# Kernel optimization log

Hardware: AMD Instinct MI355X
Metric: run time of the kernel (lower is better)

## Reference

```python
import jax, jax.numpy as jnp
import numpy as np

DM = 512      # d_model
DM4 = DM // 4 # per-modality embed dim
DI = 2 * DM   # d_inner (expand=2)
DS = 16       # d_state
DTR = 32      # dt_rank = d_model/16
DC = 4        # d_conv
NL = 3        # n_layers
SD = 17       # state_dim
AD = 7        # act_dim
MAXT = 2048   # max_ep_len
EPS = 1e-5


def setup_inputs() -> dict:
    key = jax.random.key(0)
    ks = jax.random.split(key, 32)
    B, L = 2, 1024
    f32 = jnp.float32

    def rn(k, shape, s=0.02):
        return jax.random.normal(k, shape, f32) * s

    inp = {}
    inp["states"] = jax.random.normal(ks[0], (B, L, SD), f32)
    inp["actions"] = jax.random.normal(ks[1], (B, L, AD), f32)
    inp["returns_to_go"] = jax.random.normal(ks[2], (B, L, 1), f32)
    inp["constraints_to_go"] = jax.random.normal(ks[3], (B, L, 1), f32)
    inp["timesteps"] = jax.random.randint(ks[4], (B, L), 0, MAXT)

    # embedding heads
    inp["W_s"] = rn(ks[5], (DM4, SD)); inp["b_s"] = jnp.zeros((DM4,), f32)
    inp["W_a"] = rn(ks[6], (DM4, AD)); inp["b_a"] = jnp.zeros((DM4,), f32)
    inp["W_r"] = rn(ks[7], (DM4, 1));  inp["b_r"] = jnp.zeros((DM4,), f32)
    inp["W_c"] = rn(ks[8], (DM4, 1));  inp["b_c"] = jnp.zeros((DM4,), f32)
    inp["E_t"] = rn(ks[9], (MAXT, DM4))

    # per-layer Mamba params (stacked on leading layer dim)
    inp["ln_g"] = jnp.ones((NL, DM), f32)
    inp["ln_b"] = jnp.zeros((NL, DM), f32)
    inp["in_w"] = rn(ks[10], (NL, 2 * DI, DM))
    inp["conv_w"] = rn(ks[11], (NL, DI, DC), 0.1)
    inp["conv_b"] = jnp.zeros((NL, DI), f32)
    inp["xproj_w"] = rn(ks[12], (NL, DTR + 2 * DS, DI))
    inp["dtproj_w"] = rn(ks[13], (NL, DI, DTR), 0.1)
    inp["dtproj_b"] = jnp.full((NL, DI), -4.6, f32)  # softplus^-1(~0.01)
    inp["A_log"] = jnp.log(jnp.broadcast_to(jnp.arange(1, DS + 1, dtype=f32), (NL, DI, DS)))
    inp["D_ssm"] = jnp.ones((NL, DI), f32)
    inp["out_w"] = rn(ks[14], (NL, DM, DI))

    inp["fn_g"] = jnp.ones((DM,), f32)
    inp["fn_b"] = jnp.zeros((DM,), f32)
    inp["W_ps"] = rn(ks[15], (SD, DM4)); inp["b_ps"] = jnp.zeros((SD,), f32)
    inp["W_pa"] = rn(ks[16], (AD, DM4)); inp["b_pa"] = jnp.zeros((AD,), f32)
    return inp


def _layernorm(x, g, b):
    mu = x.mean(-1, keepdims=True)
    v = ((x - mu) ** 2).mean(-1, keepdims=True)
    return (x - mu) * jax.lax.rsqrt(v + EPS) * g + b


def _mamba_mixer(x, in_w, conv_w, conv_b, xproj_w, dtproj_w, dtproj_b, A_log, Dv, out_w):
    B, L, _ = x.shape
    xz = jnp.einsum('bld,ed->ble', x, in_w)          # (B,L,2*DI)
    xc, z = jnp.split(xz, 2, axis=-1)
    # causal depthwise conv1d, kernel DC
    xp = jnp.pad(xc, ((0, 0), (DC - 1, 0), (0, 0)))
    xc = sum(xp[:, k:k + L, :] * conv_w[:, k] for k in range(DC)) + conv_b
    xc = jax.nn.silu(xc)
    xdbl = jnp.einsum('bld,ed->ble', xc, xproj_w)    # (B,L,DTR+2*DS)
    dt_low = xdbl[..., :DTR]
    Bm = xdbl[..., DTR:DTR + DS]
    Cm = xdbl[..., DTR + DS:]
    dt = jax.nn.softplus(jnp.einsum('blr,dr->bld', dt_low, dtproj_w) + dtproj_b)
    A = -jnp.exp(A_log)                               # (DI,DS)

    def step(h, xs):
        dt_t, B_t, C_t, u_t = xs                      # (B,DI),(B,DS),(B,DS),(B,DI)
        dA = jnp.exp(dt_t[:, :, None] * A)            # (B,DI,DS)
        h = h * dA + (dt_t * u_t)[:, :, None] * B_t[:, None, :]
        y = jnp.einsum('bds,bs->bd', h, C_t)
        return h, y

    h0 = jnp.zeros((B, DI, DS), x.dtype)
    xs = (dt.transpose(1, 0, 2), Bm.transpose(1, 0, 2), Cm.transpose(1, 0, 2), xc.transpose(1, 0, 2))
    _, ys = jax.lax.scan(step, h0, xs)               # (L,B,DI)
    y = ys.transpose(1, 0, 2) + Dv * xc
    y = y * jax.nn.silu(z)
    return jnp.einsum('bld,ed->ble', y, out_w)


def reference(states, actions, returns_to_go, constraints_to_go, timesteps,
              W_s, b_s, W_a, b_a, W_r, b_r, W_c, b_c, E_t,
              ln_g, ln_b, in_w, conv_w, conv_b, xproj_w, dtproj_w, dtproj_b,
              A_log, D_ssm, out_w, fn_g, fn_b, W_ps, b_ps, W_pa, b_pa):
    B, L = timesteps.shape
    te = E_t[timesteps]                               # (B,L,DM4)
    se = states @ W_s.T + b_s + te
    ae = actions @ W_a.T + b_a + te
    re = returns_to_go @ W_r.T + b_r + te
    ce = constraints_to_go @ W_c.T + b_c + te
    # shift actions right by one, zero at t=0
    ae = jnp.concatenate([jnp.zeros_like(ae[:, :1]), ae[:, :-1]], axis=1)
    x = jnp.stack((re, ce, se, ae), axis=2).reshape(B, L, 4 * DM4)  # (B,L,DM)
    for i in range(NL):
        x = x + _mamba_mixer(_layernorm(x, ln_g[i], ln_b[i]),
                             in_w[i], conv_w[i], conv_b[i], xproj_w[i],
                             dtproj_w[i], dtproj_b[i], A_log[i], D_ssm[i], out_w[i])
    x = _layernorm(x, fn_g, fn_b)
    out = x.reshape(B, L, 4, DM4)
    state_preds = out[:, :, 3] @ W_ps.T + b_ps
    action_preds = out[:, :, 2] @ W_pa.T + b_pa
    return (state_preds, action_preds)
```

## Files before the change

kernel.cpp:

```cpp
#include <hip/hip_runtime.h>
#include <cstdint>
#include <cstddef>

#define DMf 512
#define DM4 128
#define DIi 1024
#define DSs 16
#define DTRr 32
#define NLl 3
#define SDd 17
#define ADd 7
#define Bb 2
#define Ll 1024
#define NTOK (Bb*Ll)
#define CL 32
#define NCH 32

typedef __bf16 bf16x8 __attribute__((ext_vector_type(8)));
typedef float f32x4 __attribute__((ext_vector_type(4)));

__device__ inline unsigned short f2bf(float f){
  unsigned int u = __float_as_uint(f);
  unsigned int r = (u + 0x7FFFu + ((u>>16)&1u)) >> 16;
  return (unsigned short)r;
}
__device__ inline float silu_f(float v){ return v / (1.0f + __expf(-v)); }

__global__ __launch_bounds__(256) void cast_bf16_k(const float* __restrict__ src,
    unsigned short* __restrict__ dst, int n){
  int i = blockIdx.x*256 + threadIdx.x;
  if (i < n) dst[i] = f2bf(src[i]);
}

__global__ __launch_bounds__(128) void embed_k(
    const float* __restrict__ st, const float* __restrict__ ac,
    const float* __restrict__ rtg, const float* __restrict__ ctg,
    const int* __restrict__ ts,
    const float* __restrict__ Ws, const float* __restrict__ bs,
    const float* __restrict__ Wa, const float* __restrict__ ba,
    const float* __restrict__ Wr, const float* __restrict__ br,
    const float* __restrict__ Wc, const float* __restrict__ bc,
    const float* __restrict__ Et, float* __restrict__ x)
{
  int tok = blockIdx.x; int j = threadIdx.x;
  int l = tok & (Ll-1);
  int t = ts[tok];
  float te = Et[(size_t)t*DM4 + j];
  float re = rtg[tok]*Wr[j] + br[j] + te;
  float ce = ctg[tok]*Wc[j] + bc[j] + te;
  float se = bs[j] + te;
  #pragma unroll
  for (int k=0;k<SDd;++k) se += st[(size_t)tok*SDd+k]*Ws[j*SDd+k];
  float ae = 0.0f;
  if (l > 0) {
    int tp = ts[tok-1];
    ae = ba[j] + Et[(size_t)tp*DM4 + j];
    #pragma unroll
    for (int k=0;k<ADd;++k) ae += ac[(size_t)(tok-1)*ADd+k]*Wa[j*ADd+k];
  }
  float* xt = x + (size_t)tok*DMf;
  xt[0*DM4+j]=re; xt[1*DM4+j]=ce; xt[2*DM4+j]=se; xt[3*DM4+j]=ae;
}

__global__ __launch_bounds__(256) void ln_k(const float* __restrict__ x,
    const float* __restrict__ g, const float* __restrict__ bta,
    unsigned short* __restrict__ xn)
{
  int wave = threadIdx.x >> 6, lane = threadIdx.x & 63;
  int tok = blockIdx.x*4 + wave;
  const float* xr = x + (size_t)tok*DMf;
  float v[8];
  float4 a = *(const float4*)&xr[lane*8];
  float4 b = *(const float4*)&xr[lane*8+4];
  v[0]=a.x; v[1]=a.y; v[2]=a.z; v[3]=a.w; v[4]=b.x; v[5]=b.y; v[6]=b.z; v[7]=b.w;
  float s = 0.f;
  #pragma unroll
  for (int j=0;j<8;++j) s += v[j];
  #pragma unroll
  for (int m=32;m>=1;m>>=1) s += __shfl_xor(s, m, 64);
  float mu = s * (1.0f/DMf);
  float vs = 0.f;
  #pragma unroll
  for (int j=0;j<8;++j){ float d = v[j]-mu; vs += d*d; }
  #pragma unroll
  for (int m=32;m>=1;m>>=1) vs += __shfl_xor(vs, m, 64);
  float rstd = rsqrtf(vs*(1.0f/DMf) + 1e-5f);
  unsigned int o[8];
  #pragma unroll
  for (int j=0;j<8;++j){
    int c = lane*8+j;
    o[j] = f2bf((v[j]-mu)*rstd*g[c] + bta[c]);
  }
  uint4 w;
  w.x = o[0] | (o[1]<<16); w.y = o[2] | (o[3]<<16);
  w.z = o[4] | (o[5]<<16); w.w = o[6] | (o[7]<<16);
  *(uint4*)&xn[(size_t)tok*DMf + lane*8] = w;
}

template<int ACCUM>
__global__ __launch_bounds__(256) void gemm_bt_k(const unsigned short* __restrict__ A,
    const unsigned short* __restrict__ Bm, float* __restrict__ C, int M, int N, int K)
{
  __shared__ unsigned short As[128*32];
  __shared__ unsigned short Bs[128*32];
  int tid = threadIdx.x;
  int bm = blockIdx.x, bn = blockIdx.y;
  size_t row0 = (size_t)bm*128, col0 = (size_t)bn*128;
  int wave = tid>>6, lane = tid&63;
  int wr = wave>>1, wc = wave&1;
  f32x4 acc[4][4];
  f32x4 z4 = {0.f,0.f,0.f,0.f};
  #pragma unroll
  for (int m=0;m<4;++m)
    #pragma unroll
    for (int n=0;n<4;++n) acc[m][n] = z4;
  int lrow = lane&15, lko = (lane>>4)*8;
  for (int k0=0; k0<K; k0+=32){
    #pragma unroll
    for (int r=0;r<2;++r){
      int flat = r*256 + tid;
      int arow = flat>>2, ak = (flat&3)*8;
      const unsigned short* ga = A + (row0+arow)*K + k0 + ak;
      const unsigned short* gb = Bm + (col0+arow)*K + k0 + ak;
      __builtin_amdgcn_global_load_lds((const __attribute__((address_space(1))) void*)ga,
          (__attribute__((address_space(3))) void*)(&As[flat*8]), 16, 0, 0);
      __builtin_amdgcn_global_load_lds((const __attribute__((address_space(1))) void*)gb,
          (__attribute__((address_space(3))) void*)(&Bs[flat*8]), 16, 0, 0);
    }
    __syncthreads();
    bf16x8 af[4], bfv[4];
    #pragma unroll
    for (int m=0;m<4;++m) af[m] = *(const bf16x8*)&As[(wr*64+m*16+lrow)*32 + lko];
    #pragma unroll
    for (int n=0;n<4;++n) bfv[n] = *(const bf16x8*)&Bs[(wc*64+n*16+lrow)*32 + lko];
    #pragma unroll
    for (int m=0;m<4;++m)
      #pragma unroll
      for (int n=0;n<4;++n)
        acc[m][n] = __builtin_amdgcn_mfma_f32_16x16x32_bf16(af[m], bfv[n], acc[m][n], 0, 0, 0);
    __syncthreads();
  }
  int lcol = lane&15, lr4 = (lane>>4)*4;
  #pragma unroll
  for (int m=0;m<4;++m)
    #pragma unroll
    for (int n=0;n<4;++n){
      size_t row = row0 + wr*64 + m*16 + lr4;
      size_t col = col0 + wc*64 + n*16 + lcol;
      #pragma unroll
      for (int j=0;j<4;++j){
        float vv = acc[m][n][j];
        float* p = &C[(row+j)*N + col];
        if (ACCUM) *p += vv; else *p = vv;
      }
    }
}

__global__ __launch_bounds__(256) void gemm_bt64_k(const unsigned short* __restrict__ A,
    const unsigned short* __restrict__ Bm, float* __restrict__ C, int M, int N, int K)
{
  __shared__ unsigned short As[64*32];
  __shared__ unsigned short Bs[64*32];
  int tid = threadIdx.x;
  size_t row0 = (size_t)blockIdx.x*64, col0 = (size_t)blockIdx.y*64;
  int wave = tid>>6, lane = tid&63;
  int wr = wave>>1, wc = wave&1;
  f32x4 acc[2][2];
  f32x4 z4 = {0.f,0.f,0.f,0.f};
  acc[0][0]=z4; acc[0][1]=z4; acc[1][0]=z4; acc[1][1]=z4;
  int lrow = lane&15, lko = (lane>>4)*8;
  int srow = tid>>2, sk = (tid&3)*8;
  for (int k0=0; k0<K; k0+=32){
    const unsigned short* ga = A + (row0+srow)*K + k0 + sk;
    const unsigned short* gb = Bm + (col0+srow)*K + k0 + sk;
    __builtin_amdgcn_global_load_lds((const __attribute__((address_space(1))) void*)ga,
        (__attribute__((address_space(3))) void*)(&As[tid*8]), 16, 0, 0);
    __builtin_amdgcn_global_load_lds((const __attribute__((address_space(1))) void*)gb,
        (__attribute__((address_space(3))) void*)(&Bs[tid*8]), 16, 0, 0);
    __syncthreads();
    bf16x8 af[2], bfv[2];
    #pragma unroll
    for (int m=0;m<2;++m) af[m] = *(const bf16x8*)&As[(wr*32+m*16+lrow)*32 + lko];
    #pragma unroll
    for (int n=0;n<2;++n) bfv[n] = *(const bf16x8*)&Bs[(wc*32+n*16+lrow)*32 + lko];
    #pragma unroll
    for (int m=0;m<2;++m)
      #pragma unroll
      for (int n=0;n<2;++n)
        acc[m][n] = __builtin_amdgcn_mfma_f32_16x16x32_bf16(af[m], bfv[n], acc[m][n], 0, 0, 0);
    __syncthreads();
  }
  int lcol = lane&15, lr4 = (lane>>4)*4;
  #pragma unroll
  for (int m=0;m<2;++m)
    #pragma unroll
    for (int n=0;n<2;++n){
      size_t row = row0 + wr*32 + m*16 + lr4;
      size_t col = col0 + wc*32 + n*16 + lcol;
      #pragma unroll
      for (int j=0;j<4;++j)
        C[(row+j)*N + col] += acc[m][n][j];
    }
}

__global__ __launch_bounds__(256) void conv_k(const float* __restrict__ xz,
    const float* __restrict__ cw, const float* __restrict__ cb,
    float* __restrict__ xc, unsigned short* __restrict__ xcbf)
{
  int idx = blockIdx.x*256 + threadIdx.x;
  int d = idx & (DIi-1); int tok = idx >> 10; int l = tok & (Ll-1);
  float acc = cb[d];
  #pragma unroll
  for (int k=0;k<4;++k){
    int ll = l + k - 3;
    if (ll >= 0) acc += xz[(size_t)(tok + k - 3)*(2*DIi) + d] * cw[d*4+k];
  }
  float v = silu_f(acc);
  xc[idx] = v;
  xcbf[idx] = f2bf(v);
}

__global__ __launch_bounds__(256) void xproj_mfma_k(const unsigned short* __restrict__ A,
    const unsigned short* __restrict__ Bw, float* __restrict__ xdbl)
{
  __shared__ unsigned short As[64*32];
  __shared__ unsigned short Bs[64*32];
  int tid = threadIdx.x;
  size_t row0 = (size_t)blockIdx.x*64;
  int wave = tid>>6, lane = tid&63;
  int wr = wave>>1, wc = wave&1;
  f32x4 acc[2][2];
  f32x4 z4 = {0.f,0.f,0.f,0.f};
  acc[0][0]=z4; acc[0][1]=z4; acc[1][0]=z4; acc[1][1]=z4;
  int lrow = lane&15, lko = (lane>>4)*8;
  int srow = tid>>2, sk = (tid&3)*8;
  for (int k0=0; k0<DIi; k0+=32){
    const unsigned short* ga = A + (row0+srow)*DIi + k0 + sk;
    const unsigned short* gb = Bw + (size_t)srow*DIi + k0 + sk;
    __builtin_amdgcn_global_load_lds((const __attribute__((address_space(1))) void*)ga,
        (__attribute__((address_space(3))) void*)(&As[tid*8]), 16, 0, 0);
    __builtin_amdgcn_global_load_lds((const __attribute__((address_space(1))) void*)gb,
        (__attribute__((address_space(3))) void*)(&Bs[tid*8]), 16, 0, 0);
    __syncthreads();
    bf16x8 af[2], bfv[2];
    #pragma unroll
    for (int m=0;m<2;++m) af[m] = *(const bf16x8*)&As[(wr*32+m*16+lrow)*32 + lko];
    #pragma unroll
    for (int n=0;n<2;++n) bfv[n] = *(const bf16x8*)&Bs[(wc*32+n*16+lrow)*32 + lko];
    #pragma unroll
    for (int m=0;m<2;++m)
      #pragma unroll
      for (int n=0;n<2;++n)
        acc[m][n] = __builtin_amdgcn_mfma_f32_16x16x32_bf16(af[m], bfv[n], acc[m][n], 0, 0, 0);
    __syncthreads();
  }
  int lcol = lane&15, lr4 = (lane>>4)*4;
  #pragma unroll
  for (int m=0;m<2;++m)
    #pragma unroll
    for (int n=0;n<2;++n){
      size_t row = row0 + wr*32 + m*16 + lr4;
      int col = wc*32 + n*16 + lcol;
      #pragma unroll
      for (int j=0;j<4;++j)
        xdbl[(row+j)*64 + col] = acc[m][n][j];
    }
}

__global__ __launch_bounds__(256) void dtproj_k(const float* __restrict__ xdbl,
    const float* __restrict__ dw, const float* __restrict__ db, float* __restrict__ dt)
{
  int bid = blockIdx.x;
  int tok0 = (bid >> 2) * 8;
  int o = (bid & 3)*256 + threadIdx.x;
  __shared__ float lows[8][32];
  {
    int tt = threadIdx.x >> 5, kk = threadIdx.x & 31;
    lows[tt][kk] = xdbl[(size_t)(tok0+tt)*64 + kk];
  }
  __syncthreads();
  float w[32];
  #pragma unroll
  for (int q=0;q<8;++q)
    *(float4*)&w[q*4] = *(const float4*)&dw[(size_t)o*32 + q*4];
  float bias = db[o];
  #pragma unroll
  for (int t=0;t<8;++t){
    float acc = bias;
    #pragma unroll
    for (int k=0;k<32;++k) acc += w[k]*lows[t][k];
    float dv = (acc > 15.0f) ? acc : log1pf(__expf(acc));
    dt[(size_t)(tok0+t)*DIi + o] = dv;
  }
}

__global__ __launch_bounds__(256) void scan1_k(const float* __restrict__ dt,
    const float* __restrict__ xc, const float* __restrict__ xdbl,
    const float* __restrict__ Alog, float* __restrict__ Ebuf, float* __restrict__ Pbuf)
{
  int bid = blockIdx.x;
  int dblk = bid & 3; int tmp = bid >> 2; int c = tmp & (NCH-1); int b = tmp >> 5;
  int d = dblk*256 + threadIdx.x;
  float A[16], h[16], P[16];
  #pragma unroll
  for (int s=0;s<16;++s){ A[s] = -__expf(Alog[d*16+s]); h[s]=0.f; P[s]=1.f; }
  int l0 = c*CL;
  for (int l=l0; l<l0+CL; ++l){
    size_t tok = (size_t)b*Ll + l;
    float dtv = dt[tok*DIi + d];
    float u   = xc[tok*DIi + d];
    float dtu = dtv*u;
    const float* bcv = &xdbl[tok*64 + 32];
    #pragma unroll
    for (int s=0;s<16;++s){
      float dA = __expf(dtv*A[s]);
      h[s] = h[s]*dA + dtu*bcv[s];
      P[s] *= dA;
    }
  }
  size_t base = (((size_t)b*DIi + d)*NCH + c)*16;
  #pragma unroll
  for (int s=0;s<16;++s){ Ebuf[base+s]=h[s]; Pbuf[base+s]=P[s]; }
}

__global__ __launch_bounds__(256) void scanmid_k(const float* __restrict__ E,
    const float* __restrict__ P, float* __restrict__ H0)
{
  int gid = blockIdx.x*256 + threadIdx.x;
  int s = gid & 15; size_t bd = (size_t)(gid >> 4);
  float H = 0.f;
  for (int c=0;c<NCH;++c){
    size_t idx = (bd*NCH + c)*16 + s;
    H0[idx] = H;
    H = P[idx]*H + E[idx];
  }
}

__global__ __launch_bounds__(256) void scan2_k(const float* __restrict__ dt,
    const float* __restrict__ xc, const float* __restrict__ xdbl,
    const float* __restrict__ Alog, const float* __restrict__ Dv,
    const float* __restrict__ xz, const float* __restrict__ H0,
    unsigned short* __restrict__ ybf)
{
  int bid = blockIdx.x;
  int dblk = bid & 3; int tmp = bid >> 2; int c = tmp & (NCH-1); int b = tmp >> 5;
  int d = dblk*256 + threadIdx.x;
  size_t base = (((size_t)b*DIi + d)*NCH + c)*16;
  float A[16], h[16];
  #pragma unroll
  for (int s=0;s<16;++s){ A[s] = -__expf(Alog[d*16+s]); h[s] = H0[base+s]; }
  float Dd = Dv[d];
  int l0 = c*CL;
  for (int l=l0; l<l0+CL; ++l){
    size_t tok = (size_t)b*Ll + l;
    float dtv = dt[tok*DIi + d];
    float u   = xc[tok*DIi + d];
    float dtu = dtv*u;
    const float* bcv = &xdbl[tok*64 + 32];
    float y = 0.f;
    #pragma unroll
    for (int s=0;s<16;++s){
      float dA = __expf(dtv*A[s]);
      h[s] = h[s]*dA + dtu*bcv[s];
      y += h[s]*bcv[16+s];
    }
    float zv = xz[tok*(2*DIi) + DIi + d];
    ybf[tok*DIi + d] = f2bf((y + Dd*u) * silu_f(zv));
  }
}

__global__ __launch_bounds__(256) void head_k(const float* __restrict__ x,
    const float* __restrict__ g, const float* __restrict__ bta,
    const float* __restrict__ Wps, const float* __restrict__ bps,
    const float* __restrict__ Wpa, const float* __restrict__ bpa,
    float* __restrict__ out)
{
  __shared__ float lds[4][256];
  int wave = threadIdx.x >> 6, lane = threadIdx.x & 63;
  int tok = blockIdx.x*4 + wave;
  const float* xr = x + (size_t)tok*DMf;
  float v[8];
  float4 a = *(const float4*)&xr[lane*8];
  float4 b = *(const float4*)&xr[lane*8+4];
  v[0]=a.x; v[1]=a.y; v[2]=a.z; v[3]=a.w; v[4]=b.x; v[5]=b.y; v[6]=b.z; v[7]=b.w;
  float s = 0.f;
  #pragma unroll
  for (int j=0;j<8;++j) s += v[j];
  #pragma unroll
  for (int m=32;m>=1;m>>=1) s += __shfl_xor(s, m, 64);
  float mu = s * (1.0f/DMf);
  float vs = 0.f;
  #pragma unroll
  for (int j=0;j<8;++j){ float d = v[j]-mu; vs += d*d; }
  #pragma unroll
  for (int m=32;m>=1;m>>=1) vs += __shfl_xor(vs, m, 64);
  float rstd = rsqrtf(vs*(1.0f/DMf) + 1e-5f);
  if (lane >= 32){
    #pragma unroll
    for (int j=0;j<8;++j){
      int cdx = lane*8+j;
      lds[wave][cdx-256] = (v[j]-mu)*rstd*g[cdx] + bta[cdx];
    }
  }
  __syncthreads();
  if (lane < SDd){
    float acc = bps[lane];
    const float* w = &Wps[lane*DM4];
    #pragma unroll 8
    for (int k=0;k<DM4;++k) acc += lds[wave][128+k]*w[k];
    out[(size_t)tok*SDd + lane] = acc;
  } else if (lane < SDd+ADd){
    int o = lane - SDd;
    float acc = bpa[o];
    const float* w = &Wpa[o*DM4];
    #pragma unroll 8
    for (int k=0;k<DM4;++k) acc += lds[wave][k]*w[k];
    out[(size_t)NTOK*SDd + (size_t)tok*ADd + o] = acc;
  }
}

extern "C" void kernel_launch(void* const* d_in, const int* in_sizes, int n_in,
                              void* d_out, int out_size, void* d_ws, size_t ws_size,
                              hipStream_t stream)
{
  (void)in_sizes; (void)n_in; (void)out_size;
  const float* states   = (const float*)d_in[0];
  const float* actions  = (const float*)d_in[1];
  const float* rtg      = (const float*)d_in[2];
  const float* ctg      = (const float*)d_in[3];
  const int*   ts       = (const int*)d_in[4];
  const float* W_s      = (const float*)d_in[5];
  const float* b_s      = (const float*)d_in[6];
  const float* W_a      = (const float*)d_in[7];
  const float* b_a      = (const float*)d_in[8];
  const float* W_r      = (const float*)d_in[9];
  const float* b_r      = (const float*)d_in[10];
  const float* W_c      = (const float*)d_in[11];
  const float* b_c      = (const float*)d_in[12];
  const float* E_t      = (const float*)d_in[13];
  const float* ln_g     = (const float*)d_in[14];
  const float* ln_b     = (const float*)d_in[15];
  const float* in_w     = (const float*)d_in[16];
  const float* conv_w   = (const float*)d_in[17];
  const float* conv_b   = (const float*)d_in[18];
  const float* xproj_w  = (const float*)d_in[19];
  const float* dtproj_w = (const float*)d_in[20];
  const float* dtproj_b = (const float*)d_in[21];
  const float* A_log    = (const float*)d_in[22];
  const float* D_ssm    = (const float*)d_in[23];
  const float* out_w    = (const float*)d_in[24];
  const float* fn_g     = (const float*)d_in[25];
  const float* fn_b     = (const float*)d_in[26];
  const float* W_ps     = (const float*)d_in[27];
  const float* b_ps     = (const float*)d_in[28];
  const float* W_pa     = (const float*)d_in[29];
  const float* b_pa     = (const float*)d_in[30];

  char* ws = (char*)d_ws;
  constexpr size_t S_X    = (size_t)NTOK*DMf*4;
  constexpr size_t S_XN   = (size_t)NTOK*DMf*2;
  constexpr size_t S_XZ   = (size_t)NTOK*2*DIi*4;
  constexpr size_t S_XC   = (size_t)NTOK*DIi*4;
  constexpr size_t S_XCB  = (size_t)NTOK*DIi*2;
  constexpr size_t S_XDBL = (size_t)NTOK*64*4;
  constexpr size_t S_DT   = (size_t)NTOK*DIi*4;
  constexpr size_t S_YBF  = (size_t)NTOK*DIi*2;
  constexpr size_t S_INW  = (size_t)NLl*2048*512*2;
  constexpr size_t S_OUTW = (size_t)NLl*512*1024*2;
  constexpr size_t S_XPW  = (size_t)NLl*64*DIi*2;
  constexpr size_t S_E    = (size_t)Bb*DIi*NCH*16*4;
  constexpr size_t S_TOTAL = S_X+S_XN+S_XZ+S_XC+S_XCB+S_XDBL+S_DT+S_YBF
                             +S_INW+S_OUTW+S_XPW+3*S_E;

  if (ws_size < S_TOTAL) return;

  size_t off = 0;
  float* x            = (float*)(ws + off);          off += S_X;
  unsigned short* xn  = (unsigned short*)(ws + off); off += S_XN;
  float* xz           = (float*)(ws + off);          off += S_XZ;
  float* xc           = (float*)(ws + off);          off += S_XC;
  unsigned short* xcbf= (unsigned short*)(ws + off); off += S_XCB;
  float* xdbl         = (float*)(ws + off);          off += S_XDBL;
  float* dt           = (float*)(ws + off);          off += S_DT;
  unsigned short* ybf = (unsigned short*)(ws + off); off += S_YBF;
  unsigned short* inw_bf  = (unsigned short*)(ws + off); off += S_INW;
  unsigned short* outw_bf = (unsigned short*)(ws + off); off += S_OUTW;
  unsigned short* xpw_bf  = (unsigned short*)(ws + off); off += S_XPW;
  float* Ebuf         = (float*)(ws + off);          off += S_E;
  float* Pbuf         = (float*)(ws + off);          off += S_E;
  float* H0buf        = (float*)(ws + off);          off += S_E;

  const int n_inw  = NLl*2048*512;
  const int n_outw = NLl*512*1024;
  const int n_xpw  = NLl*64*DIi;
  cast_bf16_k<<<(n_inw+255)/256, 256, 0, stream>>>(in_w, inw_bf, n_inw);
  cast_bf16_k<<<(n_outw+255)/256, 256, 0, stream>>>(out_w, outw_bf, n_outw);
  cast_bf16_k<<<(n_xpw+255)/256, 256, 0, stream>>>(xproj_w, xpw_bf, n_xpw);

  embed_k<<<NTOK, 128, 0, stream>>>(states, actions, rtg, ctg, ts,
      W_s, b_s, W_a, b_a, W_r, b_r, W_c, b_c, E_t, x);

  for (int i=0;i<NLl;++i){
    ln_k<<<NTOK/4, 256, 0, stream>>>(x, ln_g + i*DMf, ln_b + i*DMf, xn);
    gemm_bt_k<0><<<dim3(NTOK/128, 2048/128), 256, 0, stream>>>(
        xn, inw_bf + (size_t)i*2048*512, xz, NTOK, 2048, 512);
    conv_k<<<(NTOK*DIi)/256, 256, 0, stream>>>(xz, conv_w + (size_t)i*DIi*4,
        conv_b + (size_t)i*DIi, xc, xcbf);
    xproj_mfma_k<<<NTOK/64, 256, 0, stream>>>(xcbf, xpw_bf + (size_t)i*64*DIi, xdbl);
    dtproj_k<<<(NTOK/8)*4, 256, 0, stream>>>(xdbl, dtproj_w + (size_t)i*DIi*32,
        dtproj_b + (size_t)i*DIi, dt);
    scan1_k<<<Bb*NCH*4, 256, 0, stream>>>(dt, xc, xdbl,
        A_log + (size_t)i*DIi*16, Ebuf, Pbuf);
    scanmid_k<<<(Bb*DIi*16)/256, 256, 0, stream>>>(Ebuf, Pbuf, H0buf);
    scan2_k<<<Bb*NCH*4, 256, 0, stream>>>(dt, xc, xdbl,
        A_log + (size_t)i*DIi*16, D_ssm + (size_t)i*DIi, xz, H0buf, ybf);
    gemm_bt64_k<<<dim3(NTOK/64, 512/64), 256, 0, stream>>>(
        ybf, outw_bf + (size_t)i*512*1024, x, NTOK, 512, 1024);
  }

  head_k<<<NTOK/4, 256, 0, stream>>>(x, fn_g, fn_b, W_ps, b_ps, W_pa, b_pa,
      (float*)d_out);
}
```

Baseline: 385.5 us.

## Fuse dt projection into scan kernels, double-buffer GEMM tiles, merge weight casts

Removes the separate dtproj kernel and the dt buffer by recomputing the dt projection and softplus inside both scan passes, so the NTOK x DI dt array is never written or re-read. All three MFMA GEMM kernels gain double-buffered LDS with explicit waitcnt and barrier-based prefetch of the next K slice, overlapping loads with compute. The three weight-cast launches merge into one kernel, and the scan chunk length halves (CL 16, NCH 64) for more parallel blocks. The trade-off is that the dt projection is computed twice, and the scan carry buffers double in size.

```diff
diff --git a/kernel.cpp b/kernel.cpp
--- a/kernel.cpp
+++ b/kernel.cpp
@@ -13,8 +13,8 @@
 #define Bb 2
 #define Ll 1024
 #define NTOK (Bb*Ll)
-#define CL 32
-#define NCH 32
+#define CL 16
+#define NCH 64
 
 typedef __bf16 bf16x8 __attribute__((ext_vector_type(8)));
 typedef float f32x4 __attribute__((ext_vector_type(4)));
@@ -26,10 +26,16 @@
 }
 __device__ inline float silu_f(float v){ return v / (1.0f + __expf(-v)); }
 
-__global__ __launch_bounds__(256) void cast_bf16_k(const float* __restrict__ src,
-    unsigned short* __restrict__ dst, int n){
+__global__ __launch_bounds__(256) void cast3_k(
+    const float* __restrict__ a, unsigned short* __restrict__ da, int na,
+    const float* __restrict__ b, unsigned short* __restrict__ db, int nb,
+    const float* __restrict__ c, unsigned short* __restrict__ dc, int nc){
   int i = blockIdx.x*256 + threadIdx.x;
-  if (i < n) dst[i] = f2bf(src[i]);
+  if (i < na) { da[i] = f2bf(a[i]); return; }
+  int j = i - na;
+  if (j < nb) { db[j] = f2bf(b[j]); return; }
+  int k = j - nb;
+  if (k < nc) dc[k] = f2bf(c[k]);
 }
 
 __global__ __launch_bounds__(128) void embed_k(
@@ -97,15 +103,27 @@
   *(uint4*)&xn[(size_t)tok*DMf + lane*8] = w;
 }
 
+#define STAGE128(buf, kk) { \
+  _Pragma("unroll") \
+  for (int r=0;r<2;++r){ \
+    int flat = r*256 + tid; \
+    int arow = flat>>2, ak = (flat&3)*8; \
+    const unsigned short* ga = A + (row0+arow)*K + (kk) + ak; \
+    const unsigned short* gb = Bm + (col0+arow)*K + (kk) + ak; \
+    __builtin_amdgcn_global_load_lds((const __attribute__((address_space(1))) void*)ga, \
+        (__attribute__((address_space(3))) void*)(&As[buf][flat*8]), 16, 0, 0); \
+    __builtin_amdgcn_global_load_lds((const __attribute__((address_space(1))) void*)gb, \
+        (__attribute__((address_space(3))) void*)(&Bs[buf][flat*8]), 16, 0, 0); \
+  } }
+
 template<int ACCUM>
 __global__ __launch_bounds__(256) void gemm_bt_k(const unsigned short* __restrict__ A,
     const unsigned short* __restrict__ Bm, float* __restrict__ C, int M, int N, int K)
 {
-  __shared__ unsigned short As[128*32];
-  __shared__ unsigned short Bs[128*32];
+  __shared__ unsigned short As[2][128*32];
+  __shared__ unsigned short Bs[2][128*32];
   int tid = threadIdx.x;
-  int bm = blockIdx.x, bn = blockIdx.y;
-  size_t row0 = (size_t)bm*128, col0 = (size_t)bn*128;
+  size_t row0 = (size_t)blockIdx.x*128, col0 = (size_t)blockIdx.y*128;
   int wave = tid>>6, lane = tid&63;
   int wr = wave>>1, wc = wave&1;
   f32x4 acc[4][4];
@@ -115,30 +133,30 @@
     #pragma unroll
     for (int n=0;n<4;++n) acc[m][n] = z4;
   int lrow = lane&15, lko = (lane>>4)*8;
-  for (int k0=0; k0<K; k0+=32){
-    #pragma unroll
-    for (int r=0;r<2;++r){
-      int flat = r*256 + tid;
-      int arow = flat>>2, ak = (flat&3)*8;
-      const unsigned short* ga = A + (row0+arow)*K + k0 + ak;
-      const unsigned short* gb = Bm + (col0+arow)*K + k0 + ak;
-      __builtin_amdgcn_global_load_lds((const __attribute__((address_space(1))) void*)ga,
-          (__attribute__((address_space(3))) void*)(&As[flat*8]), 16, 0, 0);
-      __builtin_amdgcn_global_load_lds((const __attribute__((address_space(1))) void*)gb,
-          (__attribute__((address_space(3))) void*)(&Bs[flat*8]), 16, 0, 0);
-    }
-    __syncthreads();
+  int nst = K >> 5;
+  STAGE128(0, 0);
+  for (int st=0; st<nst; ++st){
+    int cur = st & 1;
+    if (st+1 < nst){
+      STAGE128(cur^1, (st+1)*32);
+      asm volatile("s_waitcnt vmcnt(4)" ::: "memory");
+    } else {
+      asm volatile("s_waitcnt vmcnt(0)" ::: "memory");
+    }
+    __builtin_amdgcn_s_barrier();
+    __builtin_amdgcn_sched_barrier(0);
     bf16x8 af[4], bfv[4];
     #pragma unroll
-    for (int m=0;m<4;++m) af[m] = *(const bf16x8*)&As[(wr*64+m*16+lrow)*32 + lko];
-    #pragma unroll
-    for (int n=0;n<4;++n) bfv[n] = *(const bf16x8*)&Bs[(wc*64+n*16+lrow)*32 + lko];
+    for (int m=0;m<4;++m) af[m] = *(const bf16x8*)&As[cur][(wr*64+m*16+lrow)*32 + lko];
+    #pragma unroll
+    for (int n=0;n<4;++n) bfv[n] = *(const bf16x8*)&Bs[cur][(wc*64+n*16+lrow)*32 + lko];
     #pragma unroll
     for (int m=0;m<4;++m)
       #pragma unroll
       for (int n=0;n<4;++n)
         acc[m][n] = __builtin_amdgcn_mfma_f32_16x16x32_bf16(af[m], bfv[n], acc[m][n], 0, 0, 0);
-    __syncthreads();
+    __builtin_amdgcn_sched_barrier(0);
+    __builtin_amdgcn_s_barrier();
   }
   int lcol = lane&15, lr4 = (lane>>4)*4;
   #pragma unroll
@@ -156,11 +174,19 @@
     }
 }
 
+#define STAGE64(buf, kk, PB) { \
+  const unsigned short* ga = A + (row0+srow)*K + (kk) + sk; \
+  const unsigned short* gb = (PB) + (col0+srow)*K + (kk) + sk; \
+  __builtin_amdgcn_global_load_lds((const __attribute__((address_space(1))) void*)ga, \
+      (__attribute__((address_space(3))) void*)(&As[buf][tid*8]), 16, 0, 0); \
+  __builtin_amdgcn_global_load_lds((const __attribute__((address_space(1))) void*)gb, \
+      (__attribute__((address_space(3))) void*)(&Bs[buf][tid*8]), 16, 0, 0); }
+
 __global__ __launch_bounds__(256) void gemm_bt64_k(const unsigned short* __restrict__ A,
     const unsigned short* __restrict__ Bm, float* __restrict__ C, int M, int N, int K)
 {
-  __shared__ unsigned short As[64*32];
-  __shared__ unsigned short Bs[64*32];
+  __shared__ unsigned short As[2][64*32];
+  __shared__ unsigned short Bs[2][64*32];
   int tid = threadIdx.x;
   size_t row0 = (size_t)blockIdx.x*64, col0 = (size_t)blockIdx.y*64;
   int wave = tid>>6, lane = tid&63;
@@ -170,25 +196,30 @@
   acc[0][0]=z4; acc[0][1]=z4; acc[1][0]=z4; acc[1][1]=z4;
   int lrow = lane&15, lko = (lane>>4)*8;
   int srow = tid>>2, sk = (tid&3)*8;
-  for (int k0=0; k0<K; k0+=32){
-    const unsigned short* ga = A + (row0+srow)*K + k0 + sk;
-    const unsigned short* gb = Bm + (col0+srow)*K + k0 + sk;
-    __builtin_amdgcn_global_load_lds((const __attribute__((address_space(1))) void*)ga,
-        (__attribute__((address_space(3))) void*)(&As[tid*8]), 16, 0, 0);
-    __builtin_amdgcn_global_load_lds((const __attribute__((address_space(1))) void*)gb,
-        (__attribute__((address_space(3))) void*)(&Bs[tid*8]), 16, 0, 0);
-    __syncthreads();
+  int nst = K >> 5;
+  STAGE64(0, 0, Bm);
+  for (int st=0; st<nst; ++st){
+    int cur = st & 1;
+    if (st+1 < nst){
+      STAGE64(cur^1, (st+1)*32, Bm);
+      asm volatile("s_waitcnt vmcnt(2)" ::: "memory");
+    } else {
+      asm volatile("s_waitcnt vmcnt(0)" ::: "memory");
+    }
+    __builtin_amdgcn_s_barrier();
+    __builtin_amdgcn_sched_barrier(0);
     bf16x8 af[2], bfv[2];
     #pragma unroll
-    for (int m=0;m<2;++m) af[m] = *(const bf16x8*)&As[(wr*32+m*16+lrow)*32 + lko];
-    #pragma unroll
-    for (int n=0;n<2;++n) bfv[n] = *(const bf16x8*)&Bs[(wc*32+n*16+lrow)*32 + lko];
+    for (int m=0;m<2;++m) af[m] = *(const bf16x8*)&As[cur][(wr*32+m*16+lrow)*32 + lko];
+    #pragma unroll
+    for (int n=0;n<2;++n) bfv[n] = *(const bf16x8*)&Bs[cur][(wc*32+n*16+lrow)*32 + lko];
     #pragma unroll
     for (int m=0;m<2;++m)
       #pragma unroll
       for (int n=0;n<2;++n)
         acc[m][n] = __builtin_amdgcn_mfma_f32_16x16x32_bf16(af[m], bfv[n], acc[m][n], 0, 0, 0);
-    __syncthreads();
+    __builtin_amdgcn_sched_barrier(0);
+    __builtin_amdgcn_s_barrier();
   }
   int lcol = lane&15, lr4 = (lane>>4)*4;
   #pragma unroll
@@ -223,10 +254,12 @@
 __global__ __launch_bounds__(256) void xproj_mfma_k(const unsigned short* __restrict__ A,
     const unsigned short* __restrict__ Bw, float* __restrict__ xdbl)
 {
-  __shared__ unsigned short As[64*32];
-  __shared__ unsigned short Bs[64*32];
+  __shared__ unsigned short As[2][64*32];
+  __shared__ unsigned short Bs[2][64*32];
   int tid = threadIdx.x;
   size_t row0 = (size_t)blockIdx.x*64;
+  const size_t col0 = 0; const int K = DIi;
+  const unsigned short* Bm = Bw;
   int wave = tid>>6, lane = tid&63;
   int wr = wave>>1, wc = wave&1;
   f32x4 acc[2][2];
@@ -234,25 +267,30 @@
   acc[0][0]=z4; acc[0][1]=z4; acc[1][0]=z4; acc[1][1]=z4;
   int lrow = lane&15, lko = (lane>>4)*8;
   int srow = tid>>2, sk = (tid&3)*8;
-  for (int k0=0; k0<DIi; k0+=32){
-    const unsigned short* ga = A + (row0+srow)*DIi + k0 + sk;
-    const unsigned short* gb = Bw + (size_t)srow*DIi + k0 + sk;
-    __builtin_amdgcn_global_load_lds((const __attribute__((address_space(1))) void*)ga,
-        (__attribute__((address_space(3))) void*)(&As[tid*8]), 16, 0, 0);
-    __builtin_amdgcn_global_load_lds((const __attribute__((address_space(1))) void*)gb,
-        (__attribute__((address_space(3))) void*)(&Bs[tid*8]), 16, 0, 0);
-    __syncthreads();
+  int nst = K >> 5;
+  STAGE64(0, 0, Bm);
+  for (int st=0; st<nst; ++st){
+    int cur = st & 1;
+    if (st+1 < nst){
+      STAGE64(cur^1, (st+1)*32, Bm);
+      asm volatile("s_waitcnt vmcnt(2)" ::: "memory");
+    } else {
+      asm volatile("s_waitcnt vmcnt(0)" ::: "memory");
+    }
+    __builtin_amdgcn_s_barrier();
+    __builtin_amdgcn_sched_barrier(0);
     bf16x8 af[2], bfv[2];
     #pragma unroll
-    for (int m=0;m<2;++m) af[m] = *(const bf16x8*)&As[(wr*32+m*16+lrow)*32 + lko];
-    #pragma unroll
-    for (int n=0;n<2;++n) bfv[n] = *(const bf16x8*)&Bs[(wc*32+n*16+lrow)*32 + lko];
+    for (int m=0;m<2;++m) af[m] = *(const bf16x8*)&As[cur][(wr*32+m*16+lrow)*32 + lko];
+    #pragma unroll
+    for (int n=0;n<2;++n) bfv[n] = *(const bf16x8*)&Bs[cur][(wc*32+n*16+lrow)*32 + lko];
     #pragma unroll
     for (int m=0;m<2;++m)
       #pragma unroll
       for (int n=0;n<2;++n)
         acc[m][n] = __builtin_amdgcn_mfma_f32_16x16x32_bf16(af[m], bfv[n], acc[m][n], 0, 0, 0);
-    __syncthreads();
+    __builtin_amdgcn_sched_barrier(0);
+    __builtin_amdgcn_s_barrier();
   }
   int lcol = lane&15, lr4 = (lane>>4)*4;
   #pragma unroll
@@ -267,54 +305,38 @@
     }
 }
 
-__global__ __launch_bounds__(256) void dtproj_k(const float* __restrict__ xdbl,
-    const float* __restrict__ dw, const float* __restrict__ db, float* __restrict__ dt)
+__global__ __launch_bounds__(256) void scan1_k(const float* __restrict__ xc,
+    const float* __restrict__ xdbl, const float* __restrict__ dw,
+    const float* __restrict__ dbias, const float* __restrict__ Alog,
+    float* __restrict__ Ebuf, float* __restrict__ Pbuf)
 {
   int bid = blockIdx.x;
-  int tok0 = (bid >> 2) * 8;
-  int o = (bid & 3)*256 + threadIdx.x;
-  __shared__ float lows[8][32];
-  {
-    int tt = threadIdx.x >> 5, kk = threadIdx.x & 31;
-    lows[tt][kk] = xdbl[(size_t)(tok0+tt)*64 + kk];
-  }
-  __syncthreads();
+  int dblk = bid & 3; int tmp = bid >> 2; int c = tmp & (NCH-1); int b = tmp >> 6;
+  int d = dblk*256 + threadIdx.x;
   float w[32];
   #pragma unroll
-  for (int q=0;q<8;++q)
-    *(float4*)&w[q*4] = *(const float4*)&dw[(size_t)o*32 + q*4];
-  float bias = db[o];
-  #pragma unroll
-  for (int t=0;t<8;++t){
-    float acc = bias;
-    #pragma unroll
-    for (int k=0;k<32;++k) acc += w[k]*lows[t][k];
-    float dv = (acc > 15.0f) ? acc : log1pf(__expf(acc));
-    dt[(size_t)(tok0+t)*DIi + o] = dv;
-  }
-}
-
-__global__ __launch_bounds__(256) void scan1_k(const float* __restrict__ dt,
-    const float* __restrict__ xc, const float* __restrict__ xdbl,
-    const float* __restrict__ Alog, float* __restrict__ Ebuf, float* __restrict__ Pbuf)
-{
-  int bid = blockIdx.x;
-  int dblk = bid & 3; int tmp = bid >> 2; int c = tmp & (NCH-1); int b = tmp >> 5;
-  int d = dblk*256 + threadIdx.x;
+  for (int q=0;q<8;++q) *(f32x4*)&w[q*4] = *(const f32x4*)&dw[(size_t)d*32 + q*4];
+  float bias = dbias[d];
   float A[16], h[16], P[16];
   #pragma unroll
   for (int s=0;s<16;++s){ A[s] = -__expf(Alog[d*16+s]); h[s]=0.f; P[s]=1.f; }
   int l0 = c*CL;
   for (int l=l0; l<l0+CL; ++l){
     size_t tok = (size_t)b*Ll + l;
-    float dtv = dt[tok*DIi + d];
-    float u   = xc[tok*DIi + d];
+    const float* xrow = &xdbl[tok*64];
+    float acc = bias;
+    #pragma unroll
+    for (int r=0;r<32;r+=4){
+      f32x4 xv = *(const f32x4*)&xrow[r];
+      acc += w[r]*xv[0] + w[r+1]*xv[1] + w[r+2]*xv[2] + w[r+3]*xv[3];
+    }
+    float dtv = (acc > 15.0f) ? acc : log1pf(__expf(acc));
+    float u = xc[tok*DIi + d];
     float dtu = dtv*u;
-    const float* bcv = &xdbl[tok*64 + 32];
     #pragma unroll
     for (int s=0;s<16;++s){
       float dA = __expf(dtv*A[s]);
-      h[s] = h[s]*dA + dtu*bcv[s];
+      h[s] = h[s]*dA + dtu*xrow[32+s];
       P[s] *= dA;
     }
   }
@@ -336,15 +358,19 @@
   }
 }
 
-__global__ __launch_bounds__(256) void scan2_k(const float* __restrict__ dt,
-    const float* __restrict__ xc, const float* __restrict__ xdbl,
-    const float* __restrict__ Alog, const float* __restrict__ Dv,
-    const float* __restrict__ xz, const float* __restrict__ H0,
-    unsigned short* __restrict__ ybf)
+__global__ __launch_bounds__(256) void scan2_k(const float* __restrict__ xc,
+    const float* __restrict__ xdbl, const float* __restrict__ dw,
+    const float* __restrict__ dbias, const float* __restrict__ Alog,
+    const float* __restrict__ Dv, const float* __restrict__ xz,
+    const float* __restrict__ H0, unsigned short* __restrict__ ybf)
 {
   int bid = blockIdx.x;
-  int dblk = bid & 3; int tmp = bid >> 2; int c = tmp & (NCH-1); int b = tmp >> 5;
+  int dblk = bid & 3; int tmp = bid >> 2; int c = tmp & (NCH-1); int b = tmp >> 6;
   int d = dblk*256 + threadIdx.x;
+  float w[32];
+  #pragma unroll
+  for (int q=0;q<8;++q) *(f32x4*)&w[q*4] = *(const f32x4*)&dw[(size_t)d*32 + q*4];
+  float bias = dbias[d];
   size_t base = (((size_t)b*DIi + d)*NCH + c)*16;
   float A[16], h[16];
   #pragma unroll
@@ -353,16 +379,22 @@
   int l0 = c*CL;
   for (int l=l0; l<l0+CL; ++l){
     size_t tok = (size_t)b*Ll + l;
-    float dtv = dt[tok*DIi + d];
-    float u   = xc[tok*DIi + d];
+    const float* xrow = &xdbl[tok*64];
+    float acc = bias;
+    #pragma unroll
+    for (int r=0;r<32;r+=4){
+      f32x4 xv = *(const f32x4*)&xrow[r];
+      acc += w[r]*xv[0] + w[r+1]*xv[1] + w[r+2]*xv[2] + w[r+3]*xv[3];
+    }
+    float dtv = (acc > 15.0f) ? acc : log1pf(__expf(acc));
+    float u = xc[tok*DIi + d];
     float dtu = dtv*u;
-    const float* bcv = &xdbl[tok*64 + 32];
     float y = 0.f;
     #pragma unroll
     for (int s=0;s<16;++s){
       float dA = __expf(dtv*A[s]);
-      h[s] = h[s]*dA + dtu*bcv[s];
-      y += h[s]*bcv[16+s];
+      h[s] = h[s]*dA + dtu*xrow[32+s];
+      y += h[s]*xrow[48+s];
     }
     float zv = xz[tok*(2*DIi) + DIi + d];
     ybf[tok*DIi + d] = f2bf((y + Dd*u) * silu_f(zv));
@@ -463,13 +495,12 @@
   constexpr size_t S_XC   = (size_t)NTOK*DIi*4;
   constexpr size_t S_XCB  = (size_t)NTOK*DIi*2;
   constexpr size_t S_XDBL = (size_t)NTOK*64*4;
-  constexpr size_t S_DT   = (size_t)NTOK*DIi*4;
   constexpr size_t S_YBF  = (size_t)NTOK*DIi*2;
   constexpr size_t S_INW  = (size_t)NLl*2048*512*2;
   constexpr size_t S_OUTW = (size_t)NLl*512*1024*2;
   constexpr size_t S_XPW  = (size_t)NLl*64*DIi*2;
   constexpr size_t S_E    = (size_t)Bb*DIi*NCH*16*4;
-  constexpr size_t S_TOTAL = S_X+S_XN+S_XZ+S_XC+S_XCB+S_XDBL+S_DT+S_YBF
+  constexpr size_t S_TOTAL = S_X+S_XN+S_XZ+S_XC+S_XCB+S_XDBL+S_YBF
                              +S_INW+S_OUTW+S_XPW+3*S_E;
 
   if (ws_size < S_TOTAL) return;
@@ -481,7 +512,6 @@
   float* xc           = (float*)(ws + off);          off += S_XC;
   unsigned short* xcbf= (unsigned short*)(ws + off); off += S_XCB;
   float* xdbl         = (float*)(ws + off);          off += S_XDBL;
-  float* dt           = (float*)(ws + off);          off += S_DT;
   unsigned short* ybf = (unsigned short*)(ws + off); off += S_YBF;
   unsigned short* inw_bf  = (unsigned short*)(ws + off); off += S_INW;
   unsigned short* outw_bf = (unsigned short*)(ws + off); off += S_OUTW;
@@ -493,9 +523,8 @@
   const int n_inw  = NLl*2048*512;
   const int n_outw = NLl*512*1024;
   const int n_xpw  = NLl*64*DIi;
-  cast_bf16_k<<<(n_inw+255)/256, 256, 0, stream>>>(in_w, inw_bf, n_inw);
-  cast_bf16_k<<<(n_outw+255)/256, 256, 0, stream>>>(out_w, outw_bf, n_outw);
-  cast_bf16_k<<<(n_xpw+255)/256, 256, 0, stream>>>(xproj_w, xpw_bf, n_xpw);
+  cast3_k<<<(n_inw+n_outw+n_xpw+255)/256, 256, 0, stream>>>(
+      in_w, inw_bf, n_inw, out_w, outw_bf, n_outw, xproj_w, xpw_bf, n_xpw);
 
   embed_k<<<NTOK, 128, 0, stream>>>(states, actions, rtg, ctg, ts,
       W_s, b_s, W_a, b_a, W_r, b_r, W_c, b_c, E_t, x);
@@ -507,12 +536,12 @@
     conv_k<<<(NTOK*DIi)/256, 256, 0, stream>>>(xz, conv_w + (size_t)i*DIi*4,
         conv_b + (size_t)i*DIi, xc, xcbf);
     xproj_mfma_k<<<NTOK/64, 256, 0, stream>>>(xcbf, xpw_bf + (size_t)i*64*DIi, xdbl);
-    dtproj_k<<<(NTOK/8)*4, 256, 0, stream>>>(xdbl, dtproj_w + (size_t)i*DIi*32,
-        dtproj_b + (size_t)i*DIi, dt);
-    scan1_k<<<Bb*NCH*4, 256, 0, stream>>>(dt, xc, xdbl,
+    scan1_k<<<Bb*NCH*4, 256, 0, stream>>>(xc, xdbl,
+        dtproj_w + (size_t)i*DIi*32, dtproj_b + (size_t)i*DIi,
         A_log + (size_t)i*DIi*16, Ebuf, Pbuf);
     scanmid_k<<<(Bb*DIi*16)/256, 256, 0, stream>>>(Ebuf, Pbuf, H0buf);
-    scan2_k<<<Bb*NCH*4, 256, 0, stream>>>(dt, xc, xdbl,
+    scan2_k<<<Bb*NCH*4, 256, 0, stream>>>(xc, xdbl,
+        dtproj_w + (size_t)i*DIi*32, dtproj_b + (size_t)i*DIi,
         A_log + (size_t)i*DIi*16, D_ssm + (size_t)i*DIi, xz, H0buf, ybf);
     gemm_bt64_k<<<dim3(NTOK/64, 512/64), 256, 0, stream>>>(
         ybf, outw_bf + (size_t)i*512*1024, x, NTOK, 512, 1024);
```

Result: slower. 421.3 us (+9.3%).
